# Optimization experiments

Measured on AMD Instinct MI355X. Metric: run time of the kernel, lower is better.

The kernel has to match this reference:

```python
import jax, jax.numpy as jnp
import numpy as np

B, N, D, K = 16, 1024, 512, 8
NUM_ITERS = 3
EPS = 1e-08
LN_EPS = 1e-05


def layer_norm(x, g, b):
    m = jnp.mean(x, axis=-1, keepdims=True)
    v = jnp.var(x, axis=-1, keepdims=True)
    return (x - m) * jax.lax.rsqrt(v + LN_EPS) * g + b


def setup_inputs() -> dict:
    key = jax.random.key(0)
    ks = jax.random.split(key, 8)
    s = 1.0 / np.sqrt(D)
    return {
        "embeddings": jax.random.normal(ks[0], (B, N, D), jnp.float32),
        "noise_init": jax.random.normal(ks[1], (B, K, D), jnp.float32),
        "noise_final": jax.random.normal(ks[2], (B, K, D), jnp.float32),
        "slots_mu": jax.random.normal(ks[3], (1, K, D), jnp.float32) * s,
        "slots_logsigma": jax.random.normal(ks[4], (1, K, D), jnp.float32) * s,
        "mixing_coeffs": jnp.ones((1, K), jnp.float32) / K,
        "Wk": jax.random.normal(ks[5], (D, D), jnp.float32) * s,
        "bk": jnp.zeros((D,), jnp.float32),
        "Wq": jax.random.normal(ks[6], (D, D), jnp.float32) * s,
        "bq": jnp.zeros((D,), jnp.float32),
        "Wv": jax.random.normal(ks[7], (D, D), jnp.float32) * s,
        "bv": jnp.zeros((D,), jnp.float32),
        "ln_g": jnp.ones((D,), jnp.float32),
        "ln_b": jnp.zeros((D,), jnp.float32),
    }


def reference(embeddings, noise_init, noise_final, slots_mu, slots_logsigma,
              mixing_coeffs, Wk, bk, Wq, bq, Wv, bv, ln_g, ln_b):
    b, n, d = embeddings.shape
    mixing = jnp.broadcast_to(mixing_coeffs, (b, K))           # [B,K]
    mu = jnp.broadcast_to(slots_mu, (b, K, d))                 # [B,K,D]
    sigma = jnp.exp(jnp.broadcast_to(slots_logsigma, (b, K, d)))
    slots = mu + sigma * noise_init                            # sampled slots

    x = layer_norm(embeddings, ln_g, ln_b)
    keys = x @ Wk + bk                                         # [B,N,D]
    values = x @ Wv + bv                                       # [B,N,D]
    # slots are never updated inside the loop, so queries are loop-invariant
    queries = slots @ Wq + bq                                  # [B,K,D]

    log2pi = jnp.float32(np.log(2.0 * np.pi))
    attn = None
    for _ in range(NUM_ITERS):
        diff = keys[:, :, None, :] - queries[:, None, :, :]    # [B,N,K,D]
        gll = -0.5 * jnp.sum(diff * diff / (sigma[:, None] ** 2 + EPS), axis=-1)  # [B,N,K]
        gll = (-0.5 * d * log2pi
               - 0.5 * jnp.sum(jnp.log(jnp.abs(sigma) + EPS), axis=-1)[:, None, :]
               + gll)
        attn = mixing[:, None, :] * gll                        # [B,N,K]
        attn = attn / jnp.sum(attn, axis=-1, keepdims=True)
        attn = attn / (jnp.sum(attn, axis=1, keepdims=True) + EPS)
        mu = jnp.einsum('bnk,bnd->bkd', attn, values)          # [B,K,D]
        diff2 = values[:, :, None, :] - mu[:, None, :, :]      # [B,N,K,D]
        sigma = jnp.einsum('bnk,bnkd->bkd', attn, diff2 * diff2)
        mixing = jnp.sum(attn, axis=1) / n

    sigma = jnp.maximum(jnp.abs(sigma), EPS)
    slots = mu + sigma * noise_final
    return slots, jnp.transpose(attn, (0, 2, 1))
```

## Files before the change

kernel.cpp:

```cpp
#include <hip/hip_runtime.h>
#include <math.h>

#define BB 16
#define NN 1024
#define DD 512
#define KK 8
#define EPS_ 1e-8f
#define LN_EPS_ 1e-5f
#define GLL_C0 (-470.4965290007924f)

typedef __attribute__((ext_vector_type(8))) short short8;
typedef __attribute__((ext_vector_type(4))) short short4v;
typedef __attribute__((ext_vector_type(4))) float f32x4;
typedef __attribute__((ext_vector_type(4))) int int4v;

static __device__ inline short f2bf(float f) {
    unsigned u = __builtin_bit_cast(unsigned, f);
    u = (u + 0x7fff + ((u >> 16) & 1)) >> 16;
    return (short)u;
}
static __device__ inline float bf2f(short s) {
    unsigned u = ((unsigned)(unsigned short)s) << 16;
    return __builtin_bit_cast(float, u);
}

struct Params {
    const float *emb, *noise_init, *noise_final, *slots_mu, *slots_logsg,
                *mixing_co, *Wk, *bk, *Wq, *bq, *Wv, *bv, *ln_g, *ln_b;
    float *out;
    float *queries, *attn;
    float *s1c, *s2c;
    float *colsum;
    short *Abf, *Kbf, *Vbf, *WtKV, *WqT, *slotbf;
};

__global__ __launch_bounds__(256) void k_pre(Params p)
{
    __shared__ __align__(16) short eb[4352];
    int u = blockIdx.x, tid = threadIdx.x;
    if (u < 4096) {
        int row  = u * 4 + (tid >> 6);
        int lane = tid & 63;
        const float* e = p.emb + (size_t)row * DD + lane * 8;
        float4 v0 = *(const float4*)e;
        float4 v1 = *(const float4*)(e + 4);
        float v[8] = {v0.x, v0.y, v0.z, v0.w, v1.x, v1.y, v1.z, v1.w};
        float s = 0.0f;
#pragma unroll
        for (int j = 0; j < 8; j++) s += v[j];
#pragma unroll
        for (int off = 32; off; off >>= 1) s += __shfl_xor(s, off);
        float m = s * (1.0f / DD);
        float vs = 0.0f;
#pragma unroll
        for (int j = 0; j < 8; j++) { float d = v[j] - m; vs = fmaf(d, d, vs); }
#pragma unroll
        for (int off = 32; off; off >>= 1) vs += __shfl_xor(vs, off);
        float rstd = rsqrtf(vs * (1.0f / DD) + LN_EPS_);

        float4 g0 = *(const float4*)&p.ln_g[lane * 8];
        float4 g1 = *(const float4*)&p.ln_g[lane * 8 + 4];
        float4 b0 = *(const float4*)&p.ln_b[lane * 8];
        float4 b1 = *(const float4*)&p.ln_b[lane * 8 + 4];
        float g[8] = {g0.x, g0.y, g0.z, g0.w, g1.x, g1.y, g1.z, g1.w};
        float bb[8] = {b0.x, b0.y, b0.z, b0.w, b1.x, b1.y, b1.z, b1.w};
        short8 o;
#pragma unroll
        for (int j = 0; j < 8; j++) o[j] = f2bf(fmaf((v[j] - m) * rstd, g[j], bb[j]));
        *(short8*)&p.Abf[(size_t)row * DD + lane * 8] = o;
    } else if (u < 4864) {
        int idx = u - 4096;
        int z = idx >> 8, rem = idx & 255;
        const float* W = (z == 0) ? p.Wk : (z == 1) ? p.Wv : p.Wq;
        short* T; int nbase;
        if (z < 2) { T = p.WtKV; nbase = z * 512; } else { T = p.WqT; nbase = 0; }
        int k0 = (rem & 15) * 32, n0 = (rem >> 4) * 32;
        int tx = tid & 31, ty = tid >> 5;
        float (*t)[33] = (float (*)[33])eb;
#pragma unroll
        for (int q = 0; q < 4; q++)
            t[ty + q * 8][tx] = W[(size_t)(k0 + ty + q * 8) * DD + n0 + tx];
        __syncthreads();
#pragma unroll
        for (int q = 0; q < 4; q++)
            T[(size_t)(nbase + n0 + ty + q * 8) * DD + k0 + tx] = f2bf(t[tx][ty + q * 8]);
    } else {
        int idx = u - 4864;
        int b = idx >> 3, k = idx & 7;
#pragma unroll
        for (int q = 0; q < 2; q++) {
            int d = tid + q * 256;
            float sg = expf(p.slots_logsg[k * DD + d]);
            float sl = fmaf(sg, p.noise_init[((size_t)(b * KK + k)) * DD + d],
                            p.slots_mu[k * DD + d]);
            p.slotbf[((size_t)(b * KK + k)) * DD + d] = f2bf(sl);
        }
    }
}

__global__ __launch_bounds__(256) void k_gemm(Params p)
{
    __shared__ __align__(16) short smem[32768];
    int u = blockIdx.x, tid = threadIdx.x;
    int w = tid >> 6, l = tid & 63;
    int x, by, qmode;
    if (u >= 1024) {
        qmode = 1; x = u - 1024;
        if (x >= 4) {
            int gidx = (x - 4) * 256 + tid;
            for (int i = gidx; i < BB * KK * DD; i += 1024) {
                p.s1c[i] = 0.0f;
                p.s2c[i] = 0.0f;
            }
            if (gidx < BB * KK) p.colsum[gidx] = 0.0f;
            return;
        }
        by = 128;
    } else { qmode = 0; x = u >> 7; by = u & 127; }
    const short* A  = qmode ? p.slotbf : p.Abf + (size_t)by * 128 * DD;
    const short* Bt = qmode ? p.WqT : p.WtKV;
    int row0 = qmode ? 0 : by * 128;
    int col0 = x * 128;

    int sr = l >> 3;
    int sg_off = ((l & 7) ^ sr) * 8;
    int mq = (w & 1) * 64, nq = (w >> 1) * 64;
    int fr = l & 15;
    int orow = (l >> 4) * 4, ocol = l & 15;

    auto STAGE = [&](int k0, int buf) {
        short* As_ = smem + buf * 8192;
        short* Bs_ = smem + 16384 + buf * 8192;
#pragma unroll
        for (int j = 0; j < 4; j++) {
            int rbj = w * 32 + j * 8;
            int r   = rbj + sr;
            __builtin_amdgcn_global_load_lds(
                (const __attribute__((address_space(1))) unsigned int*)
                    (A + (size_t)r * DD + k0 + sg_off),
                (__attribute__((address_space(3))) unsigned int*)
                    &As_[rbj * 64 + l * 8], 16, 0, 0);
            __builtin_amdgcn_global_load_lds(
                (const __attribute__((address_space(1))) unsigned int*)
                    (Bt + (size_t)(col0 + r) * DD + k0 + sg_off),
                (__attribute__((address_space(3))) unsigned int*)
                    &Bs_[rbj * 64 + l * 8], 16, 0, 0);
        }
    };

    f32x4 acc[4][4] = {};
    STAGE(0, 0);
    __syncthreads();
    for (int i = 0; i < 8; i++) {
        if (i < 7) STAGE((i + 1) * 64, (i + 1) & 1);
        const short* As_ = smem + (i & 1) * 8192;
        const short* Bs_ = smem + 16384 + (i & 1) * 8192;
#pragma unroll
        for (int kk = 0; kk < 2; kk++) {
            int g = kk * 4 + (l >> 4);
            short8 af[4], bfv[4];
#pragma unroll
            for (int mi = 0; mi < 4; mi++)
                af[mi] = *(const short8*)&As_[(mq + mi * 16 + fr) * 64 + (g ^ (fr & 7)) * 8];
#pragma unroll
            for (int ni = 0; ni < 4; ni++)
                bfv[ni] = *(const short8*)&Bs_[(nq + ni * 16 + fr) * 64 + (g ^ (fr & 7)) * 8];
#pragma unroll
            for (int mi = 0; mi < 4; mi++)
#pragma unroll
                for (int ni = 0; ni < 4; ni++)
                    acc[mi][ni] = __builtin_amdgcn_mfma_f32_16x16x32_bf16(
                        af[mi], bfv[ni], acc[mi][ni], 0, 0, 0);
        }
        __syncthreads();
    }

    float bvv[4];
#pragma unroll
    for (int ni = 0; ni < 4; ni++) {
        int col = col0 + nq + ni * 16 + ocol;
        bvv[ni] = qmode ? p.bq[col] : (x < 4 ? p.bk[col] : p.bv[col - 512]);
    }

    if (qmode) {
#pragma unroll
        for (int ni = 0; ni < 4; ni++) {
            int col = col0 + nq + ni * 16 + ocol;
#pragma unroll
            for (int mi = 0; mi < 4; mi++)
#pragma unroll
                for (int r = 0; r < 4; r++)
                    p.queries[(size_t)(mq + mi * 16 + orow + r) * DD + col] =
                        acc[mi][ni][r] + bvv[ni];
        }
    } else {
        short* eb = smem;
        short* dst = (x < 4) ? p.Kbf : p.Vbf;
        int ccol0 = (x & 3) * 128;
#pragma unroll
        for (int mi = 0; mi < 4; mi++)
#pragma unroll
            for (int r = 0; r < 4; r++) {
                int row = mq + mi * 16 + orow + r;
                int sw = ((row >> 2) & 3) << 1;
#pragma unroll
                for (int ni = 0; ni < 4; ni++) {
                    int colg = nq + ni * 16 + ocol;
                    eb[row * 128 + (((colg >> 3) ^ sw) * 8) + (colg & 7)] =
                        f2bf(acc[mi][ni][r] + bvv[ni]);
                }
            }
        __syncthreads();
#pragma unroll
        for (int i = 0; i < 8; i++) {
            int row = i * 16 + w * 4 + (l >> 4);
            int c = l & 15;
            int cc = c ^ (((row >> 2) & 3) << 1);
            short8 vv = *(const short8*)&eb[row * 128 + cc * 8];
            *(short8*)&dst[(size_t)(row0 + row) * 512 + ccol0 + c * 8] = vv;
        }
    }
}

__global__ __launch_bounds__(512) void k_gllmu(Params p, int it)
{
    __shared__ __align__(16) short F0L[16][520];
    __shared__ __align__(16) short F1L[16][520];
    __shared__ f32x4 red[3][2][64];
    __shared__ float asml[32 * KK];
    __shared__ float off_l[16], mix_l[16];

    int u = blockIdx.x, tid = threadIdx.x;
    int w = tid >> 6, l = tid & 63;
    int b = u >> 5, chunk = u & 31;
    int n0 = chunk * 32;
    int t = w & 1, ks = w >> 1;

    if (it < 2) {
        int gidx = u * 512 + tid;
        if (gidx < BB * KK * DD) {
            p.s1c[(it + 1) * (BB * KK * DD) + gidx] = 0.0f;
            p.s2c[(it + 1) * (BB * KK * DD) + gidx] = 0.0f;
        }
        if (u == 0 && tid < BB * KK) p.colsum[(it + 1) * (BB * KK) + tid] = 0.0f;
    }

    {
        int k = w;
        const float* qrow = p.queries + ((size_t)(b * KK + k)) * DD;
        float inv = 0.0f, ssum = 0.0f;
        if (it > 0) {
            float cs = p.colsum[(it - 1) * (BB * KK) + b * KK + k];
            inv  = 1.0f / (cs + EPS_);
            ssum = cs * inv;
        }
        float c = 0.0f, ld = 0.0f;
        short8 f0v, f1v;
#pragma unroll
        for (int j = 0; j < 8; j++) {
            int d = l * 8 + j;
            float sg;
            if (it == 0) {
                sg = expf(p.slots_logsg[k * DD + d]);
            } else {
                float s1 = p.s1c[(it - 1) * (BB * KK * DD) + (b * KK + k) * DD + d];
                float s2 = p.s2c[(it - 1) * (BB * KK * DD) + (b * KK + k) * DD + d];
                float m  = s1 * inv;
                sg = s2 * inv - m * m * (2.0f - ssum);
            }
            float iv = 1.0f / (sg * sg + EPS_);
            float qv = qrow[d];
            f0v[j] = f2bf(-0.5f * iv);
            f1v[j] = f2bf(qv * iv);
            c  = fmaf(qv * qv, iv, c);
            ld += logf(fabsf(sg) + EPS_);
        }
        *(short8*)&F0L[k][l * 8] = f0v;
        *(short8*)&F1L[k][l * 8] = f1v;
        short8 zz = {};
        *(short8*)&F0L[k + 8][l * 8] = zz;
        *(short8*)&F1L[k + 8][l * 8] = zz;
#pragma unroll
        for (int m_ = 32; m_; m_ >>= 1) { c += __shfl_xor(c, m_); ld += __shfl_xor(ld, m_); }
        if (l == 0) {
            off_l[k] = GLL_C0 - 0.5f * ld - 0.5f * c;
            mix_l[k] = (it == 0) ? p.mixing_co[k] : ssum * (1.0f / NN);
            off_l[k + 8] = 0.0f;
            mix_l[k + 8] = 0.0f;
        }
    }
    __syncthreads();

    const short* Ka = p.Kbf + ((size_t)(b * NN + n0 + t * 16 + (l & 15))) * 512
                      + ks * 128 + (l >> 4) * 8;
    const short* F0r = &F0L[l & 15][ks * 128 + (l >> 4) * 8];
    const short* F1r = &F1L[l & 15][ks * 128 + (l >> 4) * 8];
    f32x4 acc0 = {}, acc1 = {};
#pragma unroll
    for (int j = 0; j < 4; j++) {
        short8 kf = *(const short8*)&Ka[j * 32];
        short8 f0 = *(const short8*)&F0r[j * 32];
        short8 f1 = *(const short8*)&F1r[j * 32];
        short8 k2;
#pragma unroll
        for (int e = 0; e < 8; e++) {
            float kv = bf2f(kf[e]);
            k2[e] = f2bf(kv * kv);
        }
        acc0 = __builtin_amdgcn_mfma_f32_16x16x32_bf16(k2, f0, acc0, 0, 0, 0);
        acc1 = __builtin_amdgcn_mfma_f32_16x16x32_bf16(kf, f1, acc1, 0, 0, 0);
    }
    f32x4 acc = acc0 + acc1;

    if (ks) red[ks - 1][t][l] = acc;
    __syncthreads();
    if (ks == 0) {
#pragma unroll
        for (int i = 0; i < 3; i++) acc += red[i][t][l];
        int col = l & 15;
        int rloc = t * 16 + (l >> 4) * 4;
        float offv = off_l[col];
        float mixv = mix_l[col];
        float a[4], den[4];
#pragma unroll
        for (int r = 0; r < 4; r++) {
            a[r] = mixv * (acc[r] + offv);
            den[r] = a[r];
        }
#pragma unroll
        for (int mask = 1; mask <= 8; mask <<= 1)
#pragma unroll
            for (int r = 0; r < 4; r++) den[r] += __shfl_xor(den[r], mask);
        float csl = 0.0f;
        if (col < KK) {
#pragma unroll
            for (int r = 0; r < 4; r++) {
                float vv = a[r] / den[r];
                asml[(rloc + r) * KK + col] = vv;
                if (it == 2)
                    p.attn[((size_t)(b * NN + n0 + rloc + r)) * KK + col] = vv;
                csl += vv;
            }
        }
        csl += __shfl_xor(csl, 16);
        csl += __shfl_xor(csl, 32);
        if (l < KK) atomicAdd(&p.colsum[it * (BB * KK) + b * KK + l], csl);
    }
    __syncthreads();

    float s1[KK] = {}, s2[KK] = {};
    const short* vb = p.Vbf + ((size_t)(b * NN + n0)) * DD + tid;
#pragma unroll 4
    for (int nn = 0; nn < 32; nn++) {
        float v = bf2f(vb[(size_t)nn * DD]);
        float vq = v * v;
        float4 a0 = *(const float4*)&asml[nn * KK];
        float4 a1 = *(const float4*)&asml[nn * KK + 4];
        float aa[8] = {a0.x, a0.y, a0.z, a0.w, a1.x, a1.y, a1.z, a1.w};
#pragma unroll
        for (int k = 0; k < KK; k++) {
            s1[k] = fmaf(aa[k], v, s1[k]);
            s2[k] = fmaf(aa[k], vq, s2[k]);
        }
    }
    float* s1d = p.s1c + it * (BB * KK * DD) + (size_t)b * KK * DD + tid;
    float* s2d = p.s2c + it * (BB * KK * DD) + (size_t)b * KK * DD + tid;
#pragma unroll
    for (int k = 0; k < KK; k++) {
        atomicAdd(&s1d[(size_t)k * DD], s1[k]);
        atomicAdd(&s2d[(size_t)k * DD], s2[k]);
    }
}

__global__ __launch_bounds__(256) void k_final(Params p)
{
    int u = blockIdx.x, tid = threadIdx.x;
    if (u < 256) {
        int gid = u * 256 + tid;
        int k = (gid >> 9) & 7;
        int b = gid >> 12;
        float s1 = p.s1c[2 * (BB * KK * DD) + gid];
        float s2 = p.s2c[2 * (BB * KK * DD) + gid];
        float cs   = p.colsum[2 * (BB * KK) + b * KK + k];
        float inv  = 1.0f / (cs + EPS_);
        float ssum = cs * inv;
        float m    = s1 * inv;
        float sg   = s2 * inv - m * m * (2.0f - ssum);
        p.out[gid] = fmaf(fmaxf(fabsf(sg), EPS_), p.noise_final[gid], m);
    } else {
        int gid = (u - 256) * 256 + tid;
        int b = gid >> 13;
        int k = (gid >> 10) & 7;
        int n = gid & 1023;
        float cs = p.colsum[2 * (BB * KK) + b * KK + k];
        p.out[BB * KK * DD + gid] =
            p.attn[((size_t)(b * NN + n)) * KK + k] / (cs + EPS_);
    }
}

extern "C" void kernel_launch(void* const* d_in, const int* in_sizes, int n_in,
                              void* d_out, int out_size, void* d_ws, size_t ws_size,
                              hipStream_t stream)
{
    Params pp;
    pp.emb         = (const float*)d_in[0];
    pp.noise_init  = (const float*)d_in[1];
    pp.noise_final = (const float*)d_in[2];
    pp.slots_mu    = (const float*)d_in[3];
    pp.slots_logsg = (const float*)d_in[4];
    pp.mixing_co   = (const float*)d_in[5];
    pp.Wk          = (const float*)d_in[6];
    pp.bk          = (const float*)d_in[7];
    pp.Wq          = (const float*)d_in[8];
    pp.bq          = (const float*)d_in[9];
    pp.Wv          = (const float*)d_in[10];
    pp.bv          = (const float*)d_in[11];
    pp.ln_g        = (const float*)d_in[12];
    pp.ln_b        = (const float*)d_in[13];
    pp.out         = (float*)d_out;

    float* ws = (float*)d_ws;
    pp.queries = ws;
    pp.attn    = pp.queries + BB * KK * DD;
    pp.s1c     = pp.attn + BB * NN * KK;
    pp.s2c     = pp.s1c + 3 * BB * KK * DD;
    pp.colsum  = pp.s2c + 3 * BB * KK * DD;
    pp.Abf     = (short*)(pp.colsum + 3 * BB * KK);
    pp.Kbf     = pp.Abf + (size_t)BB * NN * DD;
    pp.Vbf     = pp.Kbf + (size_t)BB * NN * DD;
    pp.WtKV    = pp.Vbf + (size_t)BB * NN * DD;
    pp.WqT     = pp.WtKV + (size_t)1024 * DD;
    pp.slotbf  = pp.WqT + (size_t)DD * DD;

    k_pre<<<4992, 256, 0, stream>>>(pp);
    k_gemm<<<1032, 256, 0, stream>>>(pp);
    for (int it = 0; it < 3; it++)
        k_gllmu<<<512, 512, 0, stream>>>(pp, it);
    k_final<<<768, 256, 0, stream>>>(pp);
}
```

Before: 223.0 us.

## Fuse iteration and final kernels into one persistent kernel with per-batch barriers

Replaces the three per-iteration launches and the final launch with a single kernel of 128 blocks. Each block owns 128 rows of one batch, and the blocks of a batch synchronise between iterations through an atomic counter and a spin-wait. The final outputs are written directly from shared-memory attention weights, so the attention scratch buffer is no longer written and re-read. The intent is to remove launch gaps and global round trips. In exchange, fewer blocks are in flight than there are CUs, each block does more serial work, and the spin barrier adds latency.

```diff
diff --git a/kernel.cpp b/kernel.cpp
--- a/kernel.cpp
+++ b/kernel.cpp
@@ -31,6 +31,7 @@
     float *queries, *attn;
     float *s1c, *s2c;
     float *colsum;
+    int   *cnt;
     short *Abf, *Kbf, *Vbf, *WtKV, *WqT, *slotbf;
 };
 
@@ -108,11 +109,12 @@
         qmode = 1; x = u - 1024;
         if (x >= 4) {
             int gidx = (x - 4) * 256 + tid;
-            for (int i = gidx; i < BB * KK * DD; i += 1024) {
+            for (int i = gidx; i < 3 * BB * KK * DD; i += 1024) {
                 p.s1c[i] = 0.0f;
                 p.s2c[i] = 0.0f;
             }
-            if (gidx < BB * KK) p.colsum[gidx] = 0.0f;
+            if (gidx < 3 * BB * KK) p.colsum[gidx] = 0.0f;
+            if (gidx < BB) p.cnt[gidx] = 0;
             return;
         }
         by = 128;
@@ -222,179 +224,184 @@
     }
 }
 
-__global__ __launch_bounds__(512) void k_gllmu(Params p, int it)
+__global__ __launch_bounds__(512) void k_iter(Params p)
 {
     __shared__ __align__(16) short F0L[16][520];
     __shared__ __align__(16) short F1L[16][520];
     __shared__ f32x4 red[3][2][64];
-    __shared__ float asml[32 * KK];
+    __shared__ __align__(16) float asml[128 * KK];
     __shared__ float off_l[16], mix_l[16];
 
     int u = blockIdx.x, tid = threadIdx.x;
     int w = tid >> 6, l = tid & 63;
-    int b = u >> 5, chunk = u & 31;
-    int n0 = chunk * 32;
+    int b = u >> 3, chunk = u & 7;
+    int n0 = chunk * 128;
     int t = w & 1, ks = w >> 1;
 
-    if (it < 2) {
-        int gidx = u * 512 + tid;
-        if (gidx < BB * KK * DD) {
-            p.s1c[(it + 1) * (BB * KK * DD) + gidx] = 0.0f;
-            p.s2c[(it + 1) * (BB * KK * DD) + gidx] = 0.0f;
-        }
-        if (u == 0 && tid < BB * KK) p.colsum[(it + 1) * (BB * KK) + tid] = 0.0f;
+    for (int it = 0; it < 3; it++) {
+        {
+            int k = w;
+            const float* qrow = p.queries + ((size_t)(b * KK + k)) * DD;
+            float inv = 0.0f, ssum = 0.0f;
+            if (it > 0) {
+                float cs = p.colsum[(it - 1) * (BB * KK) + b * KK + k];
+                inv  = 1.0f / (cs + EPS_);
+                ssum = cs * inv;
+            }
+            float c = 0.0f, ld = 0.0f;
+            short8 f0v, f1v;
+#pragma unroll
+            for (int j = 0; j < 8; j++) {
+                int d = l * 8 + j;
+                float sg;
+                if (it == 0) {
+                    sg = expf(p.slots_logsg[k * DD + d]);
+                } else {
+                    float s1 = p.s1c[(it - 1) * (BB * KK * DD) + (b * KK + k) * DD + d];
+                    float s2 = p.s2c[(it - 1) * (BB * KK * DD) + (b * KK + k) * DD + d];
+                    float m  = s1 * inv;
+                    sg = s2 * inv - m * m * (2.0f - ssum);
+                }
+                float iv = 1.0f / (sg * sg + EPS_);
+                float qv = qrow[d];
+                f0v[j] = f2bf(-0.5f * iv);
+                f1v[j] = f2bf(qv * iv);
+                c  = fmaf(qv * qv, iv, c);
+                ld += logf(fabsf(sg) + EPS_);
+            }
+            *(short8*)&F0L[k][l * 8] = f0v;
+            *(short8*)&F1L[k][l * 8] = f1v;
+            if (it == 0) {
+                short8 zz = {};
+                *(short8*)&F0L[k + 8][l * 8] = zz;
+                *(short8*)&F1L[k + 8][l * 8] = zz;
+            }
+#pragma unroll
+            for (int m_ = 32; m_; m_ >>= 1) { c += __shfl_xor(c, m_); ld += __shfl_xor(ld, m_); }
+            if (l == 0) {
+                off_l[k] = GLL_C0 - 0.5f * ld - 0.5f * c;
+                mix_l[k] = (it == 0) ? p.mixing_co[k] : ssum * (1.0f / NN);
+                if (it == 0) { off_l[k + 8] = 0.0f; mix_l[k + 8] = 0.0f; }
+            }
+        }
+        __syncthreads();
+
+        float csl = 0.0f;
+#pragma unroll
+        for (int st = 0; st < 4; st++) {
+            const short* Ka = p.Kbf
+                + ((size_t)(b * NN + n0 + st * 32 + t * 16 + (l & 15))) * 512
+                + ks * 128 + (l >> 4) * 8;
+            const short* F0r = &F0L[l & 15][ks * 128 + (l >> 4) * 8];
+            const short* F1r = &F1L[l & 15][ks * 128 + (l >> 4) * 8];
+            f32x4 acc0 = {}, acc1 = {};
+#pragma unroll
+            for (int j = 0; j < 4; j++) {
+                short8 kf = *(const short8*)&Ka[j * 32];
+                short8 f0 = *(const short8*)&F0r[j * 32];
+                short8 f1 = *(const short8*)&F1r[j * 32];
+                short8 k2;
+#pragma unroll
+                for (int e = 0; e < 8; e++) {
+                    float kv = bf2f(kf[e]);
+                    k2[e] = f2bf(kv * kv);
+                }
+                acc0 = __builtin_amdgcn_mfma_f32_16x16x32_bf16(k2, f0, acc0, 0, 0, 0);
+                acc1 = __builtin_amdgcn_mfma_f32_16x16x32_bf16(kf, f1, acc1, 0, 0, 0);
+            }
+            f32x4 acc = acc0 + acc1;
+            if (ks) red[ks - 1][t][l] = acc;
+            __syncthreads();
+            if (ks == 0) {
+#pragma unroll
+                for (int i = 0; i < 3; i++) acc += red[i][t][l];
+                int col = l & 15;
+                int rloc = st * 32 + t * 16 + (l >> 4) * 4;
+                float offv = off_l[col];
+                float mixv = mix_l[col];
+                float a[4], den[4];
+#pragma unroll
+                for (int r = 0; r < 4; r++) { a[r] = mixv * (acc[r] + offv); den[r] = a[r]; }
+#pragma unroll
+                for (int mask = 1; mask <= 8; mask <<= 1)
+#pragma unroll
+                    for (int r = 0; r < 4; r++) den[r] += __shfl_xor(den[r], mask);
+                if (col < KK) {
+#pragma unroll
+                    for (int r = 0; r < 4; r++) {
+                        float vv = a[r] / den[r];
+                        asml[(rloc + r) * KK + col] = vv;
+                        csl += vv;
+                    }
+                }
+            }
+            __syncthreads();
+        }
+        if (ks == 0) {
+            csl += __shfl_xor(csl, 16);
+            csl += __shfl_xor(csl, 32);
+            if (l < KK) atomicAdd(&p.colsum[it * (BB * KK) + b * KK + l], csl);
+        }
+
+        float s1[KK] = {}, s2[KK] = {};
+        const short* vb = p.Vbf + ((size_t)(b * NN + n0)) * DD + tid;
+#pragma unroll 4
+        for (int nn = 0; nn < 128; nn++) {
+            float v = bf2f(vb[(size_t)nn * DD]);
+            float vq = v * v;
+            float4 a0 = *(const float4*)&asml[nn * KK];
+            float4 a1 = *(const float4*)&asml[nn * KK + 4];
+            float aa[8] = {a0.x, a0.y, a0.z, a0.w, a1.x, a1.y, a1.z, a1.w};
+#pragma unroll
+            for (int k = 0; k < KK; k++) {
+                s1[k] = fmaf(aa[k], v, s1[k]);
+                s2[k] = fmaf(aa[k], vq, s2[k]);
+            }
+        }
+        {
+            float* s1d = p.s1c + it * (BB * KK * DD) + (size_t)b * KK * DD + tid;
+            float* s2d = p.s2c + it * (BB * KK * DD) + (size_t)b * KK * DD + tid;
+#pragma unroll
+            for (int k = 0; k < KK; k++) {
+                atomicAdd(&s1d[(size_t)k * DD], s1[k]);
+                atomicAdd(&s2d[(size_t)k * DD], s2[k]);
+            }
+        }
+
+        __threadfence();
+        __syncthreads();
+        if (tid == 0) {
+            atomicAdd(&p.cnt[b], 1);
+            int target = 8 * (it + 1);
+            while (__hip_atomic_load(&p.cnt[b], __ATOMIC_ACQUIRE,
+                                     __HIP_MEMORY_SCOPE_AGENT) < target)
+                __builtin_amdgcn_s_sleep(1);
+        }
+        __syncthreads();
+        __threadfence();
     }
 
     {
-        int k = w;
-        const float* qrow = p.queries + ((size_t)(b * KK + k)) * DD;
-        float inv = 0.0f, ssum = 0.0f;
-        if (it > 0) {
-            float cs = p.colsum[(it - 1) * (BB * KK) + b * KK + k];
-            inv  = 1.0f / (cs + EPS_);
-            ssum = cs * inv;
-        }
-        float c = 0.0f, ld = 0.0f;
-        short8 f0v, f1v;
-#pragma unroll
-        for (int j = 0; j < 8; j++) {
-            int d = l * 8 + j;
-            float sg;
-            if (it == 0) {
-                sg = expf(p.slots_logsg[k * DD + d]);
-            } else {
-                float s1 = p.s1c[(it - 1) * (BB * KK * DD) + (b * KK + k) * DD + d];
-                float s2 = p.s2c[(it - 1) * (BB * KK * DD) + (b * KK + k) * DD + d];
-                float m  = s1 * inv;
-                sg = s2 * inv - m * m * (2.0f - ssum);
-            }
-            float iv = 1.0f / (sg * sg + EPS_);
-            float qv = qrow[d];
-            f0v[j] = f2bf(-0.5f * iv);
-            f1v[j] = f2bf(qv * iv);
-            c  = fmaf(qv * qv, iv, c);
-            ld += logf(fabsf(sg) + EPS_);
-        }
-        *(short8*)&F0L[k][l * 8] = f0v;
-        *(short8*)&F1L[k][l * 8] = f1v;
-        short8 zz = {};
-        *(short8*)&F0L[k + 8][l * 8] = zz;
-        *(short8*)&F1L[k + 8][l * 8] = zz;
-#pragma unroll
-        for (int m_ = 32; m_; m_ >>= 1) { c += __shfl_xor(c, m_); ld += __shfl_xor(ld, m_); }
-        if (l == 0) {
-            off_l[k] = GLL_C0 - 0.5f * ld - 0.5f * c;
-            mix_l[k] = (it == 0) ? p.mixing_co[k] : ssum * (1.0f / NN);
-            off_l[k + 8] = 0.0f;
-            mix_l[k + 8] = 0.0f;
-        }
-    }
-    __syncthreads();
-
-    const short* Ka = p.Kbf + ((size_t)(b * NN + n0 + t * 16 + (l & 15))) * 512
-                      + ks * 128 + (l >> 4) * 8;
-    const short* F0r = &F0L[l & 15][ks * 128 + (l >> 4) * 8];
-    const short* F1r = &F1L[l & 15][ks * 128 + (l >> 4) * 8];
-    f32x4 acc0 = {}, acc1 = {};
-#pragma unroll
-    for (int j = 0; j < 4; j++) {
-        short8 kf = *(const short8*)&Ka[j * 32];
-        short8 f0 = *(const short8*)&F0r[j * 32];
-        short8 f1 = *(const short8*)&F1r[j * 32];
-        short8 k2;
-#pragma unroll
-        for (int e = 0; e < 8; e++) {
-            float kv = bf2f(kf[e]);
-            k2[e] = f2bf(kv * kv);
-        }
-        acc0 = __builtin_amdgcn_mfma_f32_16x16x32_bf16(k2, f0, acc0, 0, 0, 0);
-        acc1 = __builtin_amdgcn_mfma_f32_16x16x32_bf16(kf, f1, acc1, 0, 0, 0);
-    }
-    f32x4 acc = acc0 + acc1;
-
-    if (ks) red[ks - 1][t][l] = acc;
-    __syncthreads();
-    if (ks == 0) {
-#pragma unroll
-        for (int i = 0; i < 3; i++) acc += red[i][t][l];
-        int col = l & 15;
-        int rloc = t * 16 + (l >> 4) * 4;
-        float offv = off_l[col];
-        float mixv = mix_l[col];
-        float a[4], den[4];
-#pragma unroll
-        for (int r = 0; r < 4; r++) {
-            a[r] = mixv * (acc[r] + offv);
-            den[r] = a[r];
-        }
-#pragma unroll
-        for (int mask = 1; mask <= 8; mask <<= 1)
-#pragma unroll
-            for (int r = 0; r < 4; r++) den[r] += __shfl_xor(den[r], mask);
-        float csl = 0.0f;
-        if (col < KK) {
-#pragma unroll
-            for (int r = 0; r < 4; r++) {
-                float vv = a[r] / den[r];
-                asml[(rloc + r) * KK + col] = vv;
-                if (it == 2)
-                    p.attn[((size_t)(b * NN + n0 + rloc + r)) * KK + col] = vv;
-                csl += vv;
-            }
-        }
-        csl += __shfl_xor(csl, 16);
-        csl += __shfl_xor(csl, 32);
-        if (l < KK) atomicAdd(&p.colsum[it * (BB * KK) + b * KK + l], csl);
-    }
-    __syncthreads();
-
-    float s1[KK] = {}, s2[KK] = {};
-    const short* vb = p.Vbf + ((size_t)(b * NN + n0)) * DD + tid;
-#pragma unroll 4
-    for (int nn = 0; nn < 32; nn++) {
-        float v = bf2f(vb[(size_t)nn * DD]);
-        float vq = v * v;
-        float4 a0 = *(const float4*)&asml[nn * KK];
-        float4 a1 = *(const float4*)&asml[nn * KK + 4];
-        float aa[8] = {a0.x, a0.y, a0.z, a0.w, a1.x, a1.y, a1.z, a1.w};
-#pragma unroll
-        for (int k = 0; k < KK; k++) {
-            s1[k] = fmaf(aa[k], v, s1[k]);
-            s2[k] = fmaf(aa[k], vq, s2[k]);
-        }
-    }
-    float* s1d = p.s1c + it * (BB * KK * DD) + (size_t)b * KK * DD + tid;
-    float* s2d = p.s2c + it * (BB * KK * DD) + (size_t)b * KK * DD + tid;
-#pragma unroll
-    for (int k = 0; k < KK; k++) {
-        atomicAdd(&s1d[(size_t)k * DD], s1[k]);
-        atomicAdd(&s2d[(size_t)k * DD], s2[k]);
-    }
-}
-
-__global__ __launch_bounds__(256) void k_final(Params p)
-{
-    int u = blockIdx.x, tid = threadIdx.x;
-    if (u < 256) {
-        int gid = u * 256 + tid;
+        int gid = u * 512 + tid;
         int k = (gid >> 9) & 7;
-        int b = gid >> 12;
+        int bb_ = gid >> 12;
         float s1 = p.s1c[2 * (BB * KK * DD) + gid];
         float s2 = p.s2c[2 * (BB * KK * DD) + gid];
-        float cs   = p.colsum[2 * (BB * KK) + b * KK + k];
+        float cs   = p.colsum[2 * (BB * KK) + bb_ * KK + k];
         float inv  = 1.0f / (cs + EPS_);
         float ssum = cs * inv;
         float m    = s1 * inv;
         float sg   = s2 * inv - m * m * (2.0f - ssum);
         p.out[gid] = fmaf(fmaxf(fabsf(sg), EPS_), p.noise_final[gid], m);
-    } else {
-        int gid = (u - 256) * 256 + tid;
-        int b = gid >> 13;
-        int k = (gid >> 10) & 7;
-        int n = gid & 1023;
+    }
+#pragma unroll
+    for (int q = 0; q < 2; q++) {
+        int idx = q * 512 + tid;
+        int k  = idx >> 7;
+        int nn = idx & 127;
         float cs = p.colsum[2 * (BB * KK) + b * KK + k];
-        p.out[BB * KK * DD + gid] =
-            p.attn[((size_t)(b * NN + n)) * KK + k] / (cs + EPS_);
+        p.out[(size_t)BB * KK * DD + (size_t)b * KK * NN + (size_t)k * NN + n0 + nn] =
+            asml[nn * KK + k] / (cs + EPS_);
     }
 }
 
@@ -425,7 +432,8 @@
     pp.s1c     = pp.attn + BB * NN * KK;
     pp.s2c     = pp.s1c + 3 * BB * KK * DD;
     pp.colsum  = pp.s2c + 3 * BB * KK * DD;
-    pp.Abf     = (short*)(pp.colsum + 3 * BB * KK);
+    pp.cnt     = (int*)(pp.colsum + 3 * BB * KK);
+    pp.Abf     = (short*)(pp.cnt + 16);
     pp.Kbf     = pp.Abf + (size_t)BB * NN * DD;
     pp.Vbf     = pp.Kbf + (size_t)BB * NN * DD;
     pp.WtKV    = pp.Vbf + (size_t)BB * NN * DD;
@@ -434,7 +442,5 @@
 
     k_pre<<<4992, 256, 0, stream>>>(pp);
     k_gemm<<<1032, 256, 0, stream>>>(pp);
-    for (int it = 0; it < 3; it++)
-        k_gllmu<<<512, 512, 0, stream>>>(pp, it);
-    k_final<<<768, 256, 0, stream>>>(pp);
-}
+    k_iter<<<128, 512, 0, stream>>>(pp);
+}
```

Measured after the change: 324.0 us. +45.3%, slower.
